# Kernel tuning notes

Measured on AMD Instinct MI355X. Metric: run time of the kernel, lower is better.

Reference implementation:

```python
import jax, jax.numpy as jnp
import numpy as np

N_NODES = 100000
N_EDGES = 1600000
IN_FEATS = 128
N_HIDDEN = 128
OUT_DIM = 32
BN_EPS = 1e-5


def setup_inputs() -> dict:
    key = jax.random.key(0)
    ks = jax.random.split(key, 12)
    s = 0.05  # weight init scale
    return {
        "features": jax.random.normal(ks[0], (N_NODES, IN_FEATS), dtype=jnp.float32),
        "src": jax.random.randint(ks[1], (N_EDGES,), 0, N_NODES),
        "dst": jax.random.randint(ks[2], (N_EDGES,), 0, N_NODES),
        # layer 0: in_feats -> n_hidden
        "Ws0": jax.random.normal(ks[3], (IN_FEATS, N_HIDDEN), dtype=jnp.float32) * s,
        "Wn0": jax.random.normal(ks[4], (IN_FEATS, N_HIDDEN), dtype=jnp.float32) * s,
        "b0": jnp.zeros((N_HIDDEN,), jnp.float32),
        # layer 1: n_hidden -> n_hidden
        "Ws1": jax.random.normal(ks[5], (N_HIDDEN, N_HIDDEN), dtype=jnp.float32) * s,
        "Wn1": jax.random.normal(ks[6], (N_HIDDEN, N_HIDDEN), dtype=jnp.float32) * s,
        "b1": jnp.zeros((N_HIDDEN,), jnp.float32),
        # layer 2 (output): n_hidden -> out_dim, no activation
        "Ws2": jax.random.normal(ks[7], (N_HIDDEN, OUT_DIM), dtype=jnp.float32) * s,
        "Wn2": jax.random.normal(ks[8], (N_HIDDEN, OUT_DIM), dtype=jnp.float32) * s,
        "b2": jnp.zeros((OUT_DIM,), jnp.float32),
        # batch norms after layers 0 and 1
        "g0": jnp.ones((N_HIDDEN,), jnp.float32),
        "be0": jnp.zeros((N_HIDDEN,), jnp.float32),
        "g1": jnp.ones((N_HIDDEN,), jnp.float32),
        "be1": jnp.zeros((N_HIDDEN,), jnp.float32),
    }


def _sage_mean(h, src, dst, inv_deg, Ws, Wn, b):
    # DGL SAGEConv('mean'): fc_self(h) + fc_neigh(mean of in-neighbor feats)
    agg = jax.ops.segment_sum(h[src], dst, num_segments=N_NODES) * inv_deg
    return h @ Ws + agg @ Wn + b


def _batch_norm(h, gamma, beta):
    mu = jnp.mean(h, axis=0)
    var = jnp.var(h, axis=0)
    return (h - mu) * jax.lax.rsqrt(var + BN_EPS) * gamma + beta


def reference(features, src, dst, Ws0, Wn0, b0, Ws1, Wn1, b1, Ws2, Wn2, b2, g0, be0, g1, be1):
    ones = jnp.ones((N_EDGES,), jnp.float32)
    deg = jax.ops.segment_sum(ones, dst, num_segments=N_NODES)
    inv_deg = (1.0 / jnp.maximum(deg, 1.0))[:, None]  # [N,1]

    # layer 0: SAGEConv internal activation, then BN + external activation
    h = jax.nn.relu(_sage_mean(features, src, dst, inv_deg, Ws0, Wn0, b0))
    h = jax.nn.relu(_batch_norm(h, g0, be0))
    # layer 1 (hidden)
    h = jax.nn.relu(_sage_mean(h, src, dst, inv_deg, Ws1, Wn1, b1))
    h = jax.nn.relu(_batch_norm(h, g1, be1))
    # layer 2 (output): no activation, no BN (idx > n_hidden_layers)
    h = _sage_mean(h, src, dst, inv_deg, Ws2, Wn2, b2)

    # dgl.mean_nodes over a single graph -> [1, out_dim], then softmax over classes
    hg = jnp.mean(h, axis=0, keepdims=True)
    return jax.nn.softmax(hg, axis=1)
```

## Files before the change

kernel.cpp:

```cpp
#include <hip/hip_runtime.h>
#include <hip/hip_bf16.h>

typedef __hip_bfloat16 bf16;
typedef __hip_bfloat162 bf162;

#define NN 100000
#define NE 1600000
#define BN_EPS 1e-5f

#define BSH 8
#define NBUCK ((NN + 255) >> BSH)
#define ABLK 128
#define EPBA ((NE + ABLK - 1) / ABLK)
#define CAP 6144

struct alignas(16) bf16x8 { bf16 v[8]; };

typedef __bf16 bfrag __attribute__((ext_vector_type(8)));
typedef float f4 __attribute__((ext_vector_type(4)));

static __device__ __forceinline__ float b2f(bf16 x){ return __bfloat162float(x); }
static __device__ __forceinline__ bf16 f2b(float x){ return __float2bfloat16(x); }

__global__ __launch_bounds__(256) void k_convert(const float* __restrict__ in, bf16* __restrict__ out, int n)
{
    int i = (blockIdx.x * 256 + threadIdx.x) * 8;
    if (i + 7 < n) {
        float4 a = *(const float4*)(in + i);
        float4 b = *(const float4*)(in + i + 4);
        bf16x8 o;
        o.v[0]=f2b(a.x); o.v[1]=f2b(a.y); o.v[2]=f2b(a.z); o.v[3]=f2b(a.w);
        o.v[4]=f2b(b.x); o.v[5]=f2b(b.y); o.v[6]=f2b(b.z); o.v[7]=f2b(b.w);
        *(bf16x8*)(out + i) = o;
    }
}

__global__ __launch_bounds__(256) void k_wtrans(const float* __restrict__ W0, const float* __restrict__ W1,
                                                const float* __restrict__ W2, const float* __restrict__ W3,
                                                bf16* __restrict__ T0, bf16* __restrict__ T1,
                                                bf16* __restrict__ T2, bf16* __restrict__ T3)
{
    int m = blockIdx.x >> 6;
    int t = (blockIdx.x & 63) * 256 + threadIdx.x;
    const float* W = (m == 0) ? W0 : (m == 1) ? W1 : (m == 2) ? W2 : W3;
    bf16* T = (m == 0) ? T0 : (m == 1) ? T1 : (m == 2) ? T2 : T3;
    int n = t >> 7, k = t & 127;
    T[n * 128 + k] = f2b(W[k * 128 + n]);
}

__global__ __launch_bounds__(256) void k_pa1(const int* __restrict__ dst, const int* __restrict__ src,
                                             int* __restrict__ bucketCountD, int* __restrict__ blockBaseD,
                                             int* __restrict__ bucketCountS, int* __restrict__ blockBaseS)
{
    __shared__ int histD[NBUCK];
    __shared__ int histS[NBUCK];
    int t = threadIdx.x;
    for (int i = t; i < NBUCK; i += 256) { histD[i] = 0; histS[i] = 0; }
    __syncthreads();
    int e0 = blockIdx.x * EPBA, e1 = min(e0 + EPBA, NE);
    for (int e = e0 + t; e < e1; e += 256) {
        unsigned bd = ((unsigned)dst[e]) >> BSH;
        unsigned bs = ((unsigned)src[e]) >> BSH;
        if (bd < (unsigned)NBUCK) atomicAdd(&histD[bd], 1);
        if (bs < (unsigned)NBUCK) atomicAdd(&histS[bs], 1);
    }
    __syncthreads();
    for (int i = t; i < NBUCK; i += 256) {
        blockBaseD[blockIdx.x * NBUCK + i] = atomicAdd(&bucketCountD[i], histD[i]);
        blockBaseS[blockIdx.x * NBUCK + i] = atomicAdd(&bucketCountS[i], histS[i]);
    }
}

__global__ __launch_bounds__(512) void k_bscan2(const int* __restrict__ cntD, int* __restrict__ startD,
                                                const int* __restrict__ cntS, int* __restrict__ startS)
{
    __shared__ int sd[512];
    const int* cnt = (blockIdx.x == 0) ? cntD : cntS;
    int* start = (blockIdx.x == 0) ? startD : startS;
    int t = threadIdx.x;
    int v = (t < NBUCK) ? cnt[t] : 0;
    sd[t] = v;
    __syncthreads();
    for (int o = 1; o < 512; o <<= 1) {
        int x = (t >= o) ? sd[t - o] : 0;
        __syncthreads();
        sd[t] += x;
        __syncthreads();
    }
    if (t < NBUCK) start[t] = sd[t] - v;
    if (t == 0) start[NBUCK] = NE;
}

__global__ __launch_bounds__(256) void k_pa2(const int* __restrict__ src, const int* __restrict__ dst,
                                             const int* __restrict__ bucketStartD, const int* __restrict__ blockBaseD,
                                             const int* __restrict__ bucketStartS, const int* __restrict__ blockBaseS,
                                             uint2* __restrict__ pairsD, uint2* __restrict__ pairsS)
{
    __shared__ int baseD[NBUCK];
    __shared__ int curD[NBUCK];
    __shared__ int baseS[NBUCK];
    __shared__ int curS[NBUCK];
    int t = threadIdx.x;
    for (int i = t; i < NBUCK; i += 256) {
        baseD[i] = bucketStartD[i] + blockBaseD[blockIdx.x * NBUCK + i];
        curD[i] = 0;
        baseS[i] = bucketStartS[i] + blockBaseS[blockIdx.x * NBUCK + i];
        curS[i] = 0;
    }
    __syncthreads();
    int e0 = blockIdx.x * EPBA, e1 = min(e0 + EPBA, NE);
    for (int e = e0 + t; e < e1; e += 256) {
        int s = src[e], d = dst[e];
        unsigned bd = ((unsigned)d) >> BSH;
        if (bd < (unsigned)NBUCK) {
            int r = atomicAdd(&curD[bd], 1);
            unsigned idx = (unsigned)(baseD[bd] + r);
            if (idx < (unsigned)NE) pairsD[idx] = make_uint2((unsigned)s, (unsigned)d);
        }
        unsigned bs = ((unsigned)s) >> BSH;
        if (bs < (unsigned)NBUCK) {
            int r = atomicAdd(&curS[bs], 1);
            unsigned idx = (unsigned)(baseS[bs] + r);
            if (idx < (unsigned)NE) pairsS[idx] = make_uint2((unsigned)s, (unsigned)d);
        }
    }
}

__global__ __launch_bounds__(256) void k_pb1(const uint2* __restrict__ pairs, const int* __restrict__ bucketStart,
                                             int* __restrict__ offs, float* __restrict__ invd)
{
    __shared__ int dcnt[256];
    __shared__ int sscan[256];
    int t = threadIdx.x;
    dcnt[t] = 0;
    __syncthreads();
    int b = blockIdx.x;
    int base = b << BSH;
    int p0 = bucketStart[b], p1 = bucketStart[b + 1];
    for (int i = p0 + t; i < p1; i += 256) {
        unsigned li = pairs[i].y - (unsigned)base;
        if (li < 256u) atomicAdd(&dcnt[li], 1);
    }
    __syncthreads();
    int my = dcnt[t];
    sscan[t] = my;
    __syncthreads();
    for (int o = 1; o < 256; o <<= 1) {
        int v = (t >= o) ? sscan[t - o] : 0;
        __syncthreads();
        sscan[t] += v;
        __syncthreads();
    }
    if (base + t < NN) {
        offs[base + t] = p0 + (sscan[t] - my);
        invd[base + t] = 1.0f / (float)max(my, 1);
    }
    if (b == NBUCK - 1 && t == 0) offs[NN] = NE;
}

__global__ __launch_bounds__(256) void k_wsrc2(const uint2* __restrict__ pairsS, const int* __restrict__ bucketStartS,
                                               const float* __restrict__ invd, float* __restrict__ wsrc)
{
    __shared__ float wacc[256];
    int t = threadIdx.x;
    wacc[t] = 0.f;
    __syncthreads();
    int b = blockIdx.x;
    int base = b << BSH;
    int p0 = bucketStartS[b], p1 = bucketStartS[b + 1];
    for (int i = p0 + t; i < p1; i += 256) {
        uint2 pr = pairsS[i];
        unsigned li = pr.x - (unsigned)base;
        if (li < 256u) {
            unsigned dy = pr.y; if (dy >= (unsigned)NN) dy = 0u;
            atomicAdd(&wacc[li], invd[dy]);
        }
    }
    __syncthreads();
    if (base + t < NN) wsrc[base + t] = wacc[t];
}

__global__ __launch_bounds__(256) void k_pb2(const uint2* __restrict__ pairs, const int* __restrict__ offs,
                                             int* __restrict__ esrc)
{
    __shared__ int loffs[257];
    __shared__ int cur[256];
    __shared__ int S[CAP];
    int t = threadIdx.x;
    int b = blockIdx.x;
    int base = b << BSH;
    int nEnd = min(base + 256, NN);
    int nn = nEnd - base;
    int o0 = offs[base];
    for (int i = t; i <= nn; i += 256) loffs[i] = offs[base + i] - o0;
    cur[t] = 0;
    for (int i = t; i < CAP; i += 256) S[i] = 0;
    __syncthreads();
    int cnt = loffs[nn];
    if (cnt <= CAP) {
        for (int i = t; i < cnt; i += 256) {
            uint2 pr = pairs[o0 + i];
            unsigned li = pr.y - (unsigned)base;
            if (li > 255u) li = 255u;
            int pos = loffs[li] + atomicAdd(&cur[li], 1);
            if ((unsigned)pos >= (unsigned)cnt) pos = cnt - 1;
            S[pos] = (int)pr.x;
        }
        __syncthreads();
        for (int i = t; i < cnt; i += 256) esrc[o0 + i] = S[i];
    } else {
        for (int i = t; i < cnt; i += 256) {
            uint2 pr = pairs[o0 + i];
            unsigned li = pr.y - (unsigned)base;
            if (li > 255u) li = 255u;
            int pos = loffs[li] + atomicAdd(&cur[li], 1);
            if ((unsigned)pos >= (unsigned)cnt) pos = cnt - 1;
            esrc[o0 + pos] = (int)pr.x;
        }
    }
}

__global__ __launch_bounds__(256) void k_aggregate(const bf16* __restrict__ in, bf16* __restrict__ out,
                                                   const int* __restrict__ offs, const int* __restrict__ esrc,
                                                   const float* __restrict__ invd,
                                                   const float* __restrict__ scsh, int use_ss)
{
    int row = blockIdx.x * 4 + (threadIdx.x >> 6);
    if (row >= NN) return;
    int lane = threadIdx.x & 63;
    int grp = lane >> 4;
    int c0 = (lane & 15) * 8;
    float sc[8], sh[8];
    if (use_ss) {
#pragma unroll
        for (int j = 0; j < 8; j++) { sc[j] = scsh[c0 + j]; sh[j] = scsh[128 + c0 + j]; }
    }
    int e0 = offs[row], e1 = offs[row + 1];
    float a[8];
#pragma unroll
    for (int j = 0; j < 8; j++) a[j] = 0.f;

    int e = e0 + grp;
    for (; e + 12 < e1; e += 16) {
        int s0 = esrc[e], s1 = esrc[e + 4], s2 = esrc[e + 8], s3 = esrc[e + 12];
        bf16x8 v0 = *(const bf16x8*)&in[(size_t)s0 * 128 + c0];
        bf16x8 v1 = *(const bf16x8*)&in[(size_t)s1 * 128 + c0];
        bf16x8 v2 = *(const bf16x8*)&in[(size_t)s2 * 128 + c0];
        bf16x8 v3 = *(const bf16x8*)&in[(size_t)s3 * 128 + c0];
        if (use_ss) {
#pragma unroll
            for (int j = 0; j < 8; j++)
                a[j] += fmaxf(b2f(v0.v[j]) * sc[j] + sh[j], 0.f) + fmaxf(b2f(v1.v[j]) * sc[j] + sh[j], 0.f)
                      + fmaxf(b2f(v2.v[j]) * sc[j] + sh[j], 0.f) + fmaxf(b2f(v3.v[j]) * sc[j] + sh[j], 0.f);
        } else {
#pragma unroll
            for (int j = 0; j < 8; j++)
                a[j] += (b2f(v0.v[j]) + b2f(v1.v[j])) + (b2f(v2.v[j]) + b2f(v3.v[j]));
        }
    }
    for (; e < e1; e += 4) {
        int s0 = esrc[e];
        bf16x8 v0 = *(const bf16x8*)&in[(size_t)s0 * 128 + c0];
        if (use_ss) {
#pragma unroll
            for (int j = 0; j < 8; j++) a[j] += fmaxf(b2f(v0.v[j]) * sc[j] + sh[j], 0.f);
        } else {
#pragma unroll
            for (int j = 0; j < 8; j++) a[j] += b2f(v0.v[j]);
        }
    }
#pragma unroll
    for (int j = 0; j < 8; j++) {
        a[j] += __shfl_xor(a[j], 16);
        a[j] += __shfl_xor(a[j], 32);
    }
    if (grp == 0) {
        float id = invd[row];
        bf16x8 o;
#pragma unroll
        for (int j = 0; j < 8; j++) o.v[j] = f2b(a[j] * id);
        *(bf16x8*)&out[(size_t)row * 128 + c0] = o;
    }
}

#define GM 128
__global__ __launch_bounds__(256) void k_gemm_mfma(const bf16* __restrict__ Hs, const bf16* __restrict__ Ag,
                                                   const bf16* __restrict__ Wst, const bf16* __restrict__ Wnt,
                                                   const float* __restrict__ bias,
                                                   const float* __restrict__ scsh, int use_ss,
                                                   bf16* __restrict__ outp, float* __restrict__ bnsums)
{
    __shared__ bf16 smem[2][128][72];
    __shared__ float sredsum[128], sredsq[128];
    int t = threadIdx.x;
    int row0 = blockIdx.x * GM;
    int lane = t & 63;
    int l16 = lane & 15;
    int quad = lane >> 4;
    int m0w = (t >> 6) * 32;

    if (t < 128) { sredsum[t] = 0.f; sredsq[t] = 0.f; }

    f4 acc[2][8];
#pragma unroll
    for (int rt = 0; rt < 2; rt++)
#pragma unroll
        for (int ct = 0; ct < 8; ct++) { f4 z = {0.f, 0.f, 0.f, 0.f}; acc[rt][ct] = z; }

    for (int kc = 0; kc < 128; kc += 64) {
#pragma unroll
        for (int i = 0; i < 4; i++) {
            int f = i * 256 + t;
            int row = f >> 3;
            int col8 = (f & 7) * 8;
            int grow = row0 + row;
            bf16x8 hv, av;
            if (grow < NN) {
                hv = *(const bf16x8*)&Hs[(size_t)grow * 128 + kc + col8];
                av = *(const bf16x8*)&Ag[(size_t)grow * 128 + kc + col8];
            } else {
#pragma unroll
                for (int j = 0; j < 8; j++) { hv.v[j] = f2b(0.f); av.v[j] = f2b(0.f); }
            }
            if (use_ss) {
#pragma unroll
                for (int j = 0; j < 8; j++) {
                    int k = kc + col8 + j;
                    hv.v[j] = f2b(fmaxf(b2f(hv.v[j]) * scsh[k] + scsh[128 + k], 0.f));
                }
            }
            *(bf16x8*)&smem[0][row][col8] = hv;
            *(bf16x8*)&smem[1][row][col8] = av;
        }
        __syncthreads();
#pragma unroll
        for (int ks2 = 0; ks2 < 2; ks2++) {
            int ko = ks2 * 32 + quad * 8;
            bfrag ah0 = *(const bfrag*)&smem[0][m0w + l16][ko];
            bfrag ah1 = *(const bfrag*)&smem[0][m0w + 16 + l16][ko];
            bfrag aa0 = *(const bfrag*)&smem[1][m0w + l16][ko];
            bfrag aa1 = *(const bfrag*)&smem[1][m0w + 16 + l16][ko];
            int kg = kc + ks2 * 32 + quad * 8;
#pragma unroll
            for (int ct = 0; ct < 8; ct++) {
                bfrag bs  = *(const bfrag*)&Wst[(ct * 16 + l16) * 128 + kg];
                bfrag bnf = *(const bfrag*)&Wnt[(ct * 16 + l16) * 128 + kg];
                acc[0][ct] = __builtin_amdgcn_mfma_f32_16x16x32_bf16(ah0, bs,  acc[0][ct], 0, 0, 0);
                acc[0][ct] = __builtin_amdgcn_mfma_f32_16x16x32_bf16(aa0, bnf, acc[0][ct], 0, 0, 0);
                acc[1][ct] = __builtin_amdgcn_mfma_f32_16x16x32_bf16(ah1, bs,  acc[1][ct], 0, 0, 0);
                acc[1][ct] = __builtin_amdgcn_mfma_f32_16x16x32_bf16(aa1, bnf, acc[1][ct], 0, 0, 0);
            }
        }
        __syncthreads();
    }

    bf16 (*sout)[136] = (bf16(*)[136])&smem[0][0][0];
    float psum[8], psq[8];
#pragma unroll
    for (int ct = 0; ct < 8; ct++) {
        float bv = bias[ct * 16 + l16];
        float s = 0.f, s2 = 0.f;
#pragma unroll
        for (int rt = 0; rt < 2; rt++) {
#pragma unroll
            for (int r = 0; r < 4; r++) {
                int lrow = m0w + rt * 16 + quad * 4 + r;
                float v = fmaxf(acc[rt][ct][r] + bv, 0.f);
                sout[lrow][ct * 16 + l16] = f2b(v);
                if (row0 + lrow < NN) { s += v; s2 += v * v; }
            }
        }
        psum[ct] = s; psq[ct] = s2;
    }
#pragma unroll
    for (int ct = 0; ct < 8; ct++) {
        psum[ct] += __shfl_xor(psum[ct], 16); psum[ct] += __shfl_xor(psum[ct], 32);
        psq[ct]  += __shfl_xor(psq[ct], 16);  psq[ct]  += __shfl_xor(psq[ct], 32);
    }
    if (lane < 16) {
#pragma unroll
        for (int ct = 0; ct < 8; ct++) {
            atomicAdd(&sredsum[ct * 16 + lane], psum[ct]);
            atomicAdd(&sredsq[ct * 16 + lane],  psq[ct]);
        }
    }
    __syncthreads();
#pragma unroll
    for (int i = 0; i < 8; i++) {
        int f = i * 256 + t;
        int row = f >> 4;
        int c16 = f & 15;
        int grow = row0 + row;
        if (grow < NN)
            *(bf16x8*)&outp[(size_t)grow * 128 + c16 * 8] = *(const bf16x8*)&sout[row][c16 * 8];
    }
    if (t < 128) {
        atomicAdd(&bnsums[t], sredsum[t]);
        atomicAdd(&bnsums[128 + t], sredsq[t]);
    }
}

__global__ void k_bn_fin(const float* __restrict__ sums, const float* __restrict__ g,
                         const float* __restrict__ be, float* __restrict__ scsh)
{
    int t = threadIdx.x;
    if (t < 128) {
        float mu = sums[t] / (float)NN;
        float var = sums[128 + t] / (float)NN - mu * mu;
        float sc = g[t] * rsqrtf(var + BN_EPS);
        scsh[t] = sc;
        scsh[128 + t] = be[t] - mu * sc;
    }
}

__global__ __launch_bounds__(256) void k_l2_reduce(const bf16* __restrict__ h, const float* __restrict__ scsh,
                                                   const float* __restrict__ wsrc, float* __restrict__ ue)
{
    __shared__ float su[128], se[128];
    int t = threadIdx.x;
    if (t < 128) { su[t] = 0.f; se[t] = 0.f; }
    __syncthreads();
    int c0 = (t & 15) * 8;
    int rof = t >> 4;
    float sc[8], sh[8];
#pragma unroll
    for (int j = 0; j < 8; j++) { sc[j] = scsh[c0 + j]; sh[j] = scsh[128 + c0 + j]; }
    float u[8], es[8];
#pragma unroll
    for (int j = 0; j < 8; j++) { u[j] = 0.f; es[j] = 0.f; }
    int rpb = (NN + gridDim.x - 1) / gridDim.x;
    int r0 = blockIdx.x * rpb;
    int r1 = min(r0 + rpb, NN);
    for (int r = r0 + rof; r < r1; r += 16) {
        bf16x8 v = *(const bf16x8*)&h[(size_t)r * 128 + c0];
        float w = wsrc[r];
#pragma unroll
        for (int j = 0; j < 8; j++) {
            float x = fmaxf(b2f(v.v[j]) * sc[j] + sh[j], 0.f);
            u[j] += x; es[j] += w * x;
        }
    }
#pragma unroll
    for (int j = 0; j < 8; j++) { atomicAdd(&su[c0 + j], u[j]); atomicAdd(&se[c0 + j], es[j]); }
    __syncthreads();
    if (t < 128) { atomicAdd(&ue[t], su[t]); atomicAdd(&ue[128 + t], se[t]); }
}

__global__ void k_final(const float* __restrict__ ue, const float* __restrict__ Ws2,
                        const float* __restrict__ Wn2, const float* __restrict__ b2,
                        float* __restrict__ out)
{
    __shared__ float logit[32];
    int t = threadIdx.x;
    const float inv = 1.0f / (float)NN;
    if (t < 32) {
        float acc = b2[t];
        for (int k = 0; k < 128; k++)
            acc += (ue[k] * inv) * Ws2[k * 32 + t] + (ue[128 + k] * inv) * Wn2[k * 32 + t];
        logit[t] = acc;
    }
    __syncthreads();
    if (t < 32) {
        float m = -1e30f;
        for (int j = 0; j < 32; j++) m = fmaxf(m, logit[j]);
        float s = 0.f;
        for (int j = 0; j < 32; j++) s += expf(logit[j] - m);
        out[t] = expf(logit[t] - m) / s;
    }
}

extern "C" void kernel_launch(void* const* d_in, const int* in_sizes, int n_in,
                              void* d_out, int out_size, void* d_ws, size_t ws_size,
                              hipStream_t stream)
{
    const float* feat = (const float*)d_in[0];
    const int*   src  = (const int*)d_in[1];
    const int*   dst  = (const int*)d_in[2];
    const float* Ws0  = (const float*)d_in[3];
    const float* Wn0  = (const float*)d_in[4];
    const float* b0   = (const float*)d_in[5];
    const float* Ws1  = (const float*)d_in[6];
    const float* Wn1  = (const float*)d_in[7];
    const float* b1   = (const float*)d_in[8];
    const float* Ws2  = (const float*)d_in[9];
    const float* Wn2  = (const float*)d_in[10];
    const float* b2   = (const float*)d_in[11];
    const float* g0   = (const float*)d_in[12];
    const float* be0  = (const float*)d_in[13];
    const float* g1   = (const float*)d_in[14];
    const float* be1  = (const float*)d_in[15];

    char* p = (char*)d_ws;
    auto alloc = [&](size_t b) -> void* {
        void* r = (void*)p;
        p += (b + 255) & ~(size_t)255;
        return r;
    };
    bf16* BB     = (bf16*)alloc((size_t)NN * 128 * 2);
    bf16* A      = (bf16*)alloc((size_t)NN * 128 * 2);
    uint2* pairsS= (uint2*)alloc((size_t)NE * 8);
    int*  offs   = (int*)alloc((size_t)(NN + 1) * 4);
    float* invd  = (float*)alloc((size_t)NN * 4);
    float* wsrc  = (float*)alloc((size_t)NN * 4);
    float* bn0   = (float*)alloc(256 * 4);
    float* scsh0 = (float*)alloc(256 * 4);
    float* bn1   = (float*)alloc(256 * 4);
    float* scsh1 = (float*)alloc(256 * 4);
    float* ue    = (float*)alloc(256 * 4);
    bf16* Ws0t   = (bf16*)alloc(16384 * 2);
    bf16* Wn0t   = (bf16*)alloc(16384 * 2);
    bf16* Ws1t   = (bf16*)alloc(16384 * 2);
    bf16* Wn1t   = (bf16*)alloc(16384 * 2);
    int*  bucketCountD = (int*)alloc((NBUCK + 1) * 4);
    int*  bucketStartD = (int*)alloc((NBUCK + 1) * 4);
    int*  blockBaseD   = (int*)alloc((size_t)ABLK * NBUCK * 4);
    int*  bucketCountS = (int*)alloc((NBUCK + 1) * 4);
    int*  bucketStartS = (int*)alloc((NBUCK + 1) * 4);
    int*  blockBaseS   = (int*)alloc((size_t)ABLK * NBUCK * 4);

    uint2* pairsD = (uint2*)A;
    int* esrc = (int*)pairsS;

    hipMemsetAsync(bucketCountD, 0, (NBUCK + 1) * 4, stream);
    hipMemsetAsync(bucketCountS, 0, (NBUCK + 1) * 4, stream);
    hipMemsetAsync(bn0, 0, 256 * 4, stream);
    hipMemsetAsync(bn1, 0, 256 * 4, stream);
    hipMemsetAsync(ue, 0, 256 * 4, stream);

    const int GB = (NN + GM - 1) / GM;

    k_convert<<<(NN * 128) / (256 * 8), 256, 0, stream>>>(feat, BB, NN * 128);
    k_wtrans<<<256, 256, 0, stream>>>(Ws0, Wn0, Ws1, Wn1, Ws0t, Wn0t, Ws1t, Wn1t);

    k_pa1<<<ABLK, 256, 0, stream>>>(dst, src, bucketCountD, blockBaseD, bucketCountS, blockBaseS);
    k_bscan2<<<2, 512, 0, stream>>>(bucketCountD, bucketStartD, bucketCountS, bucketStartS);
    k_pa2<<<ABLK, 256, 0, stream>>>(src, dst, bucketStartD, blockBaseD, bucketStartS, blockBaseS, pairsD, pairsS);
    k_pb1<<<NBUCK, 256, 0, stream>>>(pairsD, bucketStartD, offs, invd);
    k_wsrc2<<<NBUCK, 256, 0, stream>>>(pairsS, bucketStartS, invd, wsrc);
    k_pb2<<<NBUCK, 256, 0, stream>>>(pairsD, offs, esrc);

    k_aggregate<<<(NN + 3) / 4, 256, 0, stream>>>(BB, A, offs, esrc, invd, nullptr, 0);
    k_gemm_mfma<<<GB, 256, 0, stream>>>(BB, A, Ws0t, Wn0t, b0, nullptr, 0, BB, bn0);
    k_bn_fin<<<1, 128, 0, stream>>>(bn0, g0, be0, scsh0);

    k_aggregate<<<(NN + 3) / 4, 256, 0, stream>>>(BB, A, offs, esrc, invd, scsh0, 1);
    k_gemm_mfma<<<GB, 256, 0, stream>>>(BB, A, Ws1t, Wn1t, b1, scsh0, 1, A, bn1);
    k_bn_fin<<<1, 128, 0, stream>>>(bn1, g1, be1, scsh1);

    k_l2_reduce<<<256, 256, 0, stream>>>(A, scsh1, wsrc, ue);
    k_final<<<1, 64, 0, stream>>>(ue, Ws2, Wn2, b2, (float*)d_out);
}
```

Before: 521.5 us.

## Gather neighbor features in FP8 and pack src-bucket edge pairs into 32 bits

Adds an FP8 copy of the node features, written by the convert kernel and by the layer-0 GEMM epilogue, and makes the aggregation kernels gather 8-byte FP8 rows instead of 16-byte BF16 rows. This halves the random-gather traffic that dominates neighbor aggregation. It also packs the src-bucketed edge pairs into one 32-bit word holding the low 8 bits of src and 24 bits of dst, which halves that buffer and the k_wsrc2 reads. The cost is a large loss of precision in the aggregated neighbor features, plus extra FP8 writes.

```diff
diff --git a/kernel.cpp b/kernel.cpp
--- a/kernel.cpp
+++ b/kernel.cpp
@@ -18,11 +18,23 @@
 
 typedef __bf16 bfrag __attribute__((ext_vector_type(8)));
 typedef float f4 __attribute__((ext_vector_type(4)));
+typedef float f2 __attribute__((ext_vector_type(2)));
 
 static __device__ __forceinline__ float b2f(bf16 x){ return __bfloat162float(x); }
 static __device__ __forceinline__ bf16 f2b(float x){ return __float2bfloat16(x); }
 
-__global__ __launch_bounds__(256) void k_convert(const float* __restrict__ in, bf16* __restrict__ out, int n)
+static __device__ __forceinline__ uint2 pk8_fp8(float x0,float x1,float x2,float x3,
+                                                float x4,float x5,float x6,float x7)
+{
+    int lo = __builtin_amdgcn_cvt_pk_fp8_f32(x0, x1, 0, 0);
+    lo = __builtin_amdgcn_cvt_pk_fp8_f32(x2, x3, lo, 1);
+    int hi = __builtin_amdgcn_cvt_pk_fp8_f32(x4, x5, 0, 0);
+    hi = __builtin_amdgcn_cvt_pk_fp8_f32(x6, x7, hi, 1);
+    return make_uint2((unsigned)lo, (unsigned)hi);
+}
+
+__global__ __launch_bounds__(256) void k_convert(const float* __restrict__ in, bf16* __restrict__ out,
+                                                 unsigned char* __restrict__ outf8, int n)
 {
     int i = (blockIdx.x * 256 + threadIdx.x) * 8;
     if (i + 7 < n) {
@@ -32,6 +44,7 @@
         o.v[0]=f2b(a.x); o.v[1]=f2b(a.y); o.v[2]=f2b(a.z); o.v[3]=f2b(a.w);
         o.v[4]=f2b(b.x); o.v[5]=f2b(b.y); o.v[6]=f2b(b.z); o.v[7]=f2b(b.w);
         *(bf16x8*)(out + i) = o;
+        *(uint2*)(outf8 + i) = pk8_fp8(a.x,a.y,a.z,a.w,b.x,b.y,b.z,b.w);
     }
 }
 
@@ -94,7 +107,7 @@
 __global__ __launch_bounds__(256) void k_pa2(const int* __restrict__ src, const int* __restrict__ dst,
                                              const int* __restrict__ bucketStartD, const int* __restrict__ blockBaseD,
                                              const int* __restrict__ bucketStartS, const int* __restrict__ blockBaseS,
-                                             uint2* __restrict__ pairsD, uint2* __restrict__ pairsS)
+                                             uint2* __restrict__ pairsD, unsigned* __restrict__ packS)
 {
     __shared__ int baseD[NBUCK];
     __shared__ int curD[NBUCK];
@@ -121,7 +134,8 @@
         if (bs < (unsigned)NBUCK) {
             int r = atomicAdd(&curS[bs], 1);
             unsigned idx = (unsigned)(baseS[bs] + r);
-            if (idx < (unsigned)NE) pairsS[idx] = make_uint2((unsigned)s, (unsigned)d);
+            if (idx < (unsigned)NE)
+                packS[idx] = (((unsigned)s & 255u) << 24) | ((unsigned)d & 0xFFFFFFu);
         }
     }
 }
@@ -158,7 +172,7 @@
     if (b == NBUCK - 1 && t == 0) offs[NN] = NE;
 }
 
-__global__ __launch_bounds__(256) void k_wsrc2(const uint2* __restrict__ pairsS, const int* __restrict__ bucketStartS,
+__global__ __launch_bounds__(256) void k_wsrc2(const unsigned* __restrict__ packS, const int* __restrict__ bucketStartS,
                                                const float* __restrict__ invd, float* __restrict__ wsrc)
 {
     __shared__ float wacc[256];
@@ -169,12 +183,11 @@
     int base = b << BSH;
     int p0 = bucketStartS[b], p1 = bucketStartS[b + 1];
     for (int i = p0 + t; i < p1; i += 256) {
-        uint2 pr = pairsS[i];
-        unsigned li = pr.x - (unsigned)base;
-        if (li < 256u) {
-            unsigned dy = pr.y; if (dy >= (unsigned)NN) dy = 0u;
-            atomicAdd(&wacc[li], invd[dy]);
-        }
+        unsigned v = packS[i];
+        unsigned li = v >> 24;
+        unsigned dy = v & 0xFFFFFFu;
+        if (dy >= (unsigned)NN) dy = 0u;
+        atomicAdd(&wacc[li], invd[dy]);
     }
     __syncthreads();
     if (base + t < NN) wsrc[base + t] = wacc[t];
@@ -220,7 +233,7 @@
     }
 }
 
-__global__ __launch_bounds__(256) void k_aggregate(const bf16* __restrict__ in, bf16* __restrict__ out,
+__global__ __launch_bounds__(256) void k_aggregate(const unsigned char* __restrict__ inf8, bf16* __restrict__ out,
                                                    const int* __restrict__ offs, const int* __restrict__ esrc,
                                                    const float* __restrict__ invd,
                                                    const float* __restrict__ scsh, int use_ss)
@@ -240,33 +253,45 @@
 #pragma unroll
     for (int j = 0; j < 8; j++) a[j] = 0.f;
 
+    auto unpack = [&](uint2 u, float* v) {
+        f2 p0 = __builtin_amdgcn_cvt_pk_f32_fp8(u.x, 0);
+        f2 p1 = __builtin_amdgcn_cvt_pk_f32_fp8(u.x, 1);
+        f2 p2 = __builtin_amdgcn_cvt_pk_f32_fp8(u.y, 0);
+        f2 p3 = __builtin_amdgcn_cvt_pk_f32_fp8(u.y, 1);
+        v[0]=p0.x; v[1]=p0.y; v[2]=p1.x; v[3]=p1.y; v[4]=p2.x; v[5]=p2.y; v[6]=p3.x; v[7]=p3.y;
+    };
+
     int e = e0 + grp;
     for (; e + 12 < e1; e += 16) {
         int s0 = esrc[e], s1 = esrc[e + 4], s2 = esrc[e + 8], s3 = esrc[e + 12];
-        bf16x8 v0 = *(const bf16x8*)&in[(size_t)s0 * 128 + c0];
-        bf16x8 v1 = *(const bf16x8*)&in[(size_t)s1 * 128 + c0];
-        bf16x8 v2 = *(const bf16x8*)&in[(size_t)s2 * 128 + c0];
-        bf16x8 v3 = *(const bf16x8*)&in[(size_t)s3 * 128 + c0];
+        uint2 u0 = *(const uint2*)&inf8[(size_t)s0 * 128 + c0];
+        uint2 u1 = *(const uint2*)&inf8[(size_t)s1 * 128 + c0];
+        uint2 u2 = *(const uint2*)&inf8[(size_t)s2 * 128 + c0];
+        uint2 u3 = *(const uint2*)&inf8[(size_t)s3 * 128 + c0];
+        float v0[8], v1[8], v2[8], v3[8];
+        unpack(u0, v0); unpack(u1, v1); unpack(u2, v2); unpack(u3, v3);
         if (use_ss) {
 #pragma unroll
             for (int j = 0; j < 8; j++)
-                a[j] += fmaxf(b2f(v0.v[j]) * sc[j] + sh[j], 0.f) + fmaxf(b2f(v1.v[j]) * sc[j] + sh[j], 0.f)
-                      + fmaxf(b2f(v2.v[j]) * sc[j] + sh[j], 0.f) + fmaxf(b2f(v3.v[j]) * sc[j] + sh[j], 0.f);
+                a[j] += fmaxf(v0[j] * sc[j] + sh[j], 0.f) + fmaxf(v1[j] * sc[j] + sh[j], 0.f)
+                      + fmaxf(v2[j] * sc[j] + sh[j], 0.f) + fmaxf(v3[j] * sc[j] + sh[j], 0.f);
         } else {
 #pragma unroll
             for (int j = 0; j < 8; j++)
-                a[j] += (b2f(v0.v[j]) + b2f(v1.v[j])) + (b2f(v2.v[j]) + b2f(v3.v[j]));
+                a[j] += (v0[j] + v1[j]) + (v2[j] + v3[j]);
         }
     }
     for (; e < e1; e += 4) {
         int s0 = esrc[e];
-        bf16x8 v0 = *(const bf16x8*)&in[(size_t)s0 * 128 + c0];
+        uint2 u0 = *(const uint2*)&inf8[(size_t)s0 * 128 + c0];
+        float v0[8];
+        unpack(u0, v0);
         if (use_ss) {
 #pragma unroll
-            for (int j = 0; j < 8; j++) a[j] += fmaxf(b2f(v0.v[j]) * sc[j] + sh[j], 0.f);
+            for (int j = 0; j < 8; j++) a[j] += fmaxf(v0[j] * sc[j] + sh[j], 0.f);
         } else {
 #pragma unroll
-            for (int j = 0; j < 8; j++) a[j] += b2f(v0.v[j]);
+            for (int j = 0; j < 8; j++) a[j] += v0[j];
         }
     }
 #pragma unroll
@@ -288,7 +313,8 @@
                                                    const bf16* __restrict__ Wst, const bf16* __restrict__ Wnt,
                                                    const float* __restrict__ bias,
                                                    const float* __restrict__ scsh, int use_ss,
-                                                   bf16* __restrict__ outp, float* __restrict__ bnsums)
+                                                   bf16* __restrict__ outp, unsigned char* __restrict__ outf8,
+                                                   float* __restrict__ bnsums)
 {
     __shared__ bf16 smem[2][128][72];
     __shared__ float sredsum[128], sredsq[128];
@@ -391,8 +417,15 @@
         int row = f >> 4;
         int c16 = f & 15;
         int grow = row0 + row;
-        if (grow < NN)
-            *(bf16x8*)&outp[(size_t)grow * 128 + c16 * 8] = *(const bf16x8*)&sout[row][c16 * 8];
+        if (grow < NN) {
+            bf16x8 ov = *(const bf16x8*)&sout[row][c16 * 8];
+            *(bf16x8*)&outp[(size_t)grow * 128 + c16 * 8] = ov;
+            if (outf8) {
+                *(uint2*)&outf8[(size_t)grow * 128 + c16 * 8] =
+                    pk8_fp8(b2f(ov.v[0]), b2f(ov.v[1]), b2f(ov.v[2]), b2f(ov.v[3]),
+                            b2f(ov.v[4]), b2f(ov.v[5]), b2f(ov.v[6]), b2f(ov.v[7]));
+            }
+        }
     }
     if (t < 128) {
         atomicAdd(&bnsums[t], sredsum[t]);
@@ -498,7 +531,8 @@
     };
     bf16* BB     = (bf16*)alloc((size_t)NN * 128 * 2);
     bf16* A      = (bf16*)alloc((size_t)NN * 128 * 2);
-    uint2* pairsS= (uint2*)alloc((size_t)NE * 8);
+    unsigned char* F8 = (unsigned char*)alloc((size_t)NN * 128);
+    unsigned* packS = (unsigned*)alloc((size_t)NE * 4);
     int*  offs   = (int*)alloc((size_t)(NN + 1) * 4);
     float* invd  = (float*)alloc((size_t)NN * 4);
     float* wsrc  = (float*)alloc((size_t)NN * 4);
@@ -519,7 +553,7 @@
     int*  blockBaseS   = (int*)alloc((size_t)ABLK * NBUCK * 4);
 
     uint2* pairsD = (uint2*)A;
-    int* esrc = (int*)pairsS;
+    int* esrc = (int*)packS;
 
     hipMemsetAsync(bucketCountD, 0, (NBUCK + 1) * 4, stream);
     hipMemsetAsync(bucketCountS, 0, (NBUCK + 1) * 4, stream);
@@ -529,22 +563,22 @@
 
     const int GB = (NN + GM - 1) / GM;
 
-    k_convert<<<(NN * 128) / (256 * 8), 256, 0, stream>>>(feat, BB, NN * 128);
+    k_convert<<<(NN * 128) / (256 * 8), 256, 0, stream>>>(feat, BB, F8, NN * 128);
     k_wtrans<<<256, 256, 0, stream>>>(Ws0, Wn0, Ws1, Wn1, Ws0t, Wn0t, Ws1t, Wn1t);
 
     k_pa1<<<ABLK, 256, 0, stream>>>(dst, src, bucketCountD, blockBaseD, bucketCountS, blockBaseS);
     k_bscan2<<<2, 512, 0, stream>>>(bucketCountD, bucketStartD, bucketCountS, bucketStartS);
-    k_pa2<<<ABLK, 256, 0, stream>>>(src, dst, bucketStartD, blockBaseD, bucketStartS, blockBaseS, pairsD, pairsS);
+    k_pa2<<<ABLK, 256, 0, stream>>>(src, dst, bucketStartD, blockBaseD, bucketStartS, blockBaseS, pairsD, packS);
     k_pb1<<<NBUCK, 256, 0, stream>>>(pairsD, bucketStartD, offs, invd);
-    k_wsrc2<<<NBUCK, 256, 0, stream>>>(pairsS, bucketStartS, invd, wsrc);
+    k_wsrc2<<<NBUCK, 256, 0, stream>>>(packS, bucketStartS, invd, wsrc);
     k_pb2<<<NBUCK, 256, 0, stream>>>(pairsD, offs, esrc);
 
-    k_aggregate<<<(NN + 3) / 4, 256, 0, stream>>>(BB, A, offs, esrc, invd, nullptr, 0);
-    k_gemm_mfma<<<GB, 256, 0, stream>>>(BB, A, Ws0t, Wn0t, b0, nullptr, 0, BB, bn0);
+    k_aggregate<<<(NN + 3) / 4, 256, 0, stream>>>(F8, A, offs, esrc, invd, nullptr, 0);
+    k_gemm_mfma<<<GB, 256, 0, stream>>>(BB, A, Ws0t, Wn0t, b0, nullptr, 0, BB, F8, bn0);
     k_bn_fin<<<1, 128, 0, stream>>>(bn0, g0, be0, scsh0);
 
-    k_aggregate<<<(NN + 3) / 4, 256, 0, stream>>>(BB, A, offs, esrc, invd, scsh0, 1);
-    k_gemm_mfma<<<GB, 256, 0, stream>>>(BB, A, Ws1t, Wn1t, b1, scsh0, 1, A, bn1);
+    k_aggregate<<<(NN + 3) / 4, 256, 0, stream>>>(F8, A, offs, esrc, invd, scsh0, 1);
+    k_gemm_mfma<<<GB, 256, 0, stream>>>(BB, A, Ws1t, Wn1t, b1, scsh0, 1, A, nullptr, bn1);
     k_bn_fin<<<1, 128, 0, stream>>>(bn1, g1, be1, scsh1);
 
     k_l2_reduce<<<256, 256, 0, stream>>>(A, scsh1, wsrc, ue);
```

New measurement: 517.2 us. No clear change (-0.8%).
